# Performance work log

Hardware: AMD Instinct MI355X
Metric: run time of the kernel (lower is better)

Reference implementation:

```python
import jax, jax.numpy as jnp
import numpy as np

D_MODEL = 1024
N_HEADS = 16
D_HEAD = D_MODEL // N_HEADS
SCALE = 1.0 / (D_HEAD ** 0.5)


def _rel_shift(t):
    # Transformer-XL relative shift: pad -> view -> slice -> view. t: [b,h,q,k]
    b, h, q, k = t.shape
    padded = jnp.pad(t, ((0, 0), (0, 0), (0, 0), (1, 0)))  # [b,h,q,k+1]
    shifted = padded.reshape(b, h, k + 1, q)[:, :, 1:, :].reshape(b, h, q, k)
    return shifted


def setup_inputs() -> dict:
    key = jax.random.key(0)
    ks = jax.random.split(key, 10)
    B, T, M = 2, 1024, 1024
    J = M + T
    inp = {
        "x": jax.random.normal(ks[0], (B, T, D_MODEL), dtype=jnp.float32),
        "memory": jax.random.normal(ks[1], (B, M, D_MODEL), dtype=jnp.float32),
        "pos_emb": jax.random.normal(ks[2], (J, D_MODEL), dtype=jnp.float32),
        # nn.Linear(d, d, bias=False) weights: y = x @ W.T, W: [out, in]
        "q_w": jax.random.normal(ks[3], (D_MODEL, D_MODEL), dtype=jnp.float32) * 0.02,
        "k_w": jax.random.normal(ks[4], (D_MODEL, D_MODEL), dtype=jnp.float32) * 0.02,
        "v_w": jax.random.normal(ks[5], (D_MODEL, D_MODEL), dtype=jnp.float32) * 0.02,
        "r_w": jax.random.normal(ks[6], (D_MODEL, D_MODEL), dtype=jnp.float32) * 0.02,
        "out_w": jax.random.normal(ks[7], (D_MODEL, D_MODEL), dtype=jnp.float32) * 0.02,
        "pos_bias_u": jax.random.normal(ks[8], (N_HEADS, D_HEAD), dtype=jnp.float32) * 0.02,
        "pos_bias_v": jax.random.normal(ks[9], (N_HEADS, D_HEAD), dtype=jnp.float32) * 0.02,
    }
    return inp


def reference(x, memory, pos_emb, q_w, k_w, v_w, r_w, out_w, pos_bias_u, pos_bias_v):
    B, T, _ = x.shape
    cat = jnp.concatenate([memory, x], axis=1)  # [B, M+T, d]
    L = cat.shape[1]

    def heads(t):  # [B, time, d] -> [B, h, time, dh]
        return t.reshape(t.shape[0], t.shape[1], N_HEADS, D_HEAD).transpose(0, 2, 1, 3)

    q = heads(x @ q_w.T)      # [B,h,T,dh]
    k = heads(cat @ k_w.T)    # [B,h,L,dh]
    v = heads(cat @ v_w.T)    # [B,h,L,dh]
    r = (pos_emb @ r_w.T).reshape(-1, N_HEADS, D_HEAD).transpose(1, 0, 2)  # [h,J,dh]

    q_u = q + pos_bias_u[None, :, None, :]
    q_v = q + pos_bias_v[None, :, None, :]

    content_score = jnp.einsum('bhqd,bhkd->bhqk', q_u, k)  # [B,h,T,L]
    rel_score = jnp.einsum('bhqd,hjd->bhqj', q_v, r)        # [B,h,T,J]
    rel_score = _rel_shift(rel_score)

    scores = (content_score + rel_score) * SCALE
    attn = jax.nn.softmax(scores, axis=-1)
    out = jnp.einsum('bhqk,bhkd->bhqd', attn, v)            # [B,h,T,dh]
    out = out.transpose(0, 2, 1, 3).reshape(B, T, N_HEADS * D_HEAD)
    return out @ out_w.T
```

## Files before the change

### kernel.cpp

```cpp
#include <hip/hip_runtime.h>


typedef unsigned short u16;
typedef unsigned int u32;
typedef short bf16x8 __attribute__((ext_vector_type(8)));
typedef float f32x4 __attribute__((ext_vector_type(4)));

#define MFMA16(a, b, c) __builtin_amdgcn_mfma_f32_16x16x32_bf16(a, b, c, 0, 0, 0)

__device__ __forceinline__ u16 f2bf(float f) {
  u32 u = __float_as_uint(f);
  u32 r = (u + 0x7fffu + ((u >> 16) & 1u)) >> 16;
  return (u16)r;
}

__device__ __forceinline__ bf16x8 cvt8(float4 a, float4 b) {
  bf16x8 r;
  r[0] = (short)f2bf(a.x); r[1] = (short)f2bf(a.y);
  r[2] = (short)f2bf(a.z); r[3] = (short)f2bf(a.w);
  r[4] = (short)f2bf(b.x); r[5] = (short)f2bf(b.y);
  r[6] = (short)f2bf(b.z); r[7] = (short)f2bf(b.w);
  return r;
}

__global__ __launch_bounds__(256, 2) void gemm_qkvr(
    const float* __restrict__ x, const float* __restrict__ mem,
    const float* __restrict__ pos,
    const float* __restrict__ qw, const float* __restrict__ kw,
    const float* __restrict__ vw, const float* __restrict__ rw,
    const float* __restrict__ bu, const float* __restrict__ bv,
    u16* __restrict__ qub, u16* __restrict__ qvb, u16* __restrict__ rbuf,
    u16* __restrict__ kbuf, u16* __restrict__ vtbuf) {
  __shared__ u16 As[128 * 32], Bs[128 * 32];
  __shared__ u16 Ep[4][16 * 72];
  const int xb = blockIdx.x;
  const int bid = (xb & 7) * 96 + (xb >> 3);
  int mode, r2;
  const float* Wsrc;
  if (bid < 128)      { mode = 0; Wsrc = qw; r2 = bid; }
  else if (bid < 256) { mode = 1; Wsrc = rw; r2 = bid - 128; }
  else if (bid < 512) { mode = 2; Wsrc = kw; r2 = bid - 256; }
  else                { mode = 3; Wsrc = vw; r2 = bid - 512; }
  const int m0 = (r2 >> 3) * 128, n0 = (r2 & 7) * 128;
  const int t = threadIdx.x, lane = t & 63, wid = t >> 6;
  const int colL = lane & 15, rg = lane >> 4;
  const int wm = (wid >> 1) * 64, wn = (wid & 1) * 64;

  const float* arow[2];
  const float* wrow[2];
  int schs[2];
#pragma unroll
  for (int pass = 0; pass < 2; ++pass) {
    int slot = t + pass * 256;
    int row = slot >> 2, ch = slot & 3;
    schs[pass] = ch ^ ((row >> 1) & 3);
    int ar = m0 + row;
    if (mode == 0) {
      int b = ar >> 10;
      arow[pass] = x + ((size_t)(b * 1024 + (ar & 1023))) * 1024;
    } else if (mode == 1) {
      arow[pass] = pos + (size_t)ar * 1024;
    } else {
      int b = ar >> 11, j = ar & 2047;
      arow[pass] = (j < 1024) ? mem + ((size_t)(b * 1024 + j)) * 1024
                              : x + ((size_t)(b * 1024 + j - 1024)) * 1024;
    }
    wrow[pass] = Wsrc + (size_t)(n0 + row) * 1024;
  }

  f32x4 acc[4][4];
  f32x4 zz = {0.f, 0.f, 0.f, 0.f};
#pragma unroll
  for (int a1 = 0; a1 < 4; ++a1)
#pragma unroll
    for (int a2 = 0; a2 < 4; ++a2) acc[a1][a2] = zz;

  float4 ra[2][2], rb[2][2];
#pragma unroll
  for (int pass = 0; pass < 2; ++pass) {
    int col = schs[pass] * 8;
    ra[pass][0] = *(const float4*)(arow[pass] + col);
    ra[pass][1] = *(const float4*)(arow[pass] + col + 4);
    rb[pass][0] = *(const float4*)(wrow[pass] + col);
    rb[pass][1] = *(const float4*)(wrow[pass] + col + 4);
  }
#pragma unroll 1
  for (int kt = 0; kt < 32; ++kt) {
    __syncthreads();
#pragma unroll
    for (int pass = 0; pass < 2; ++pass) {
      int slot = t + pass * 256;
      *(bf16x8*)(As + slot * 8) = cvt8(ra[pass][0], ra[pass][1]);
      *(bf16x8*)(Bs + slot * 8) = cvt8(rb[pass][0], rb[pass][1]);
    }
    __syncthreads();
    if (kt < 31) {
#pragma unroll
      for (int pass = 0; pass < 2; ++pass) {
        int col = (kt + 1) * 32 + schs[pass] * 8;
        ra[pass][0] = *(const float4*)(arow[pass] + col);
        ra[pass][1] = *(const float4*)(arow[pass] + col + 4);
        rb[pass][0] = *(const float4*)(wrow[pass] + col);
        rb[pass][1] = *(const float4*)(wrow[pass] + col + 4);
      }
    }
    bf16x8 af[4], bfr[4];
#pragma unroll
    for (int mi = 0; mi < 4; ++mi) {
      int r = wm + mi * 16 + colL;
      af[mi] = *(const bf16x8*)(As + r * 32 + (rg ^ ((r >> 1) & 3)) * 8);
    }
#pragma unroll
    for (int ni = 0; ni < 4; ++ni) {
      int r = wn + ni * 16 + colL;
      bfr[ni] = *(const bf16x8*)(Bs + r * 32 + (rg ^ ((r >> 1) & 3)) * 8);
    }
#pragma unroll
    for (int mi = 0; mi < 4; ++mi)
#pragma unroll
      for (int ni = 0; ni < 4; ++ni)
        acc[mi][ni] = MFMA16(af[mi], bfr[ni], acc[mi][ni]);
  }

  const float sc = 0.18033688f;
  if (mode == 3) {
    u16* Ew = &Ep[wid][0];
    const int bb = m0 >> 11;
    const int j0w = (m0 + wm) & 2047;
    const int hh = (n0 + wn) >> 6;
    const size_t vb0 = (((size_t)(bb * 16 + hh) * 32 + (j0w >> 6)) * 4) * 1024;
#pragma unroll
    for (int ni = 0; ni < 4; ++ni) {
#pragma unroll
      for (int mi = 0; mi < 4; ++mi) {
        u32 lo = (u32)f2bf(acc[mi][ni][0]) | ((u32)f2bf(acc[mi][ni][1]) << 16);
        u32 hi = (u32)f2bf(acc[mi][ni][2]) | ((u32)f2bf(acc[mi][ni][3]) << 16);
        uint2 pk; pk.x = lo; pk.y = hi;
        *(uint2*)(Ew + colL * 72 + mi * 16 + rg * 4) = pk;
      }
      asm volatile("s_waitcnt lgkmcnt(0)" ::: "memory");
      const size_t vb = vb0 + (size_t)ni * 1024;
#pragma unroll
      for (int rr = 0; rr < 2; ++rr) {
        int ch = rr * 4 + rg;
        bf16x8 vv = *(const bf16x8*)(Ew + colL * 72 + ch * 8);
        *(bf16x8*)(vtbuf + vb + ch * 128 + colL * 8) = vv;
      }
      asm volatile("s_waitcnt lgkmcnt(0)" ::: "memory");
    }
    return;
  }
#pragma unroll
  for (int mi = 0; mi < 4; ++mi)
#pragma unroll
    for (int ni = 0; ni < 4; ++ni)
#pragma unroll
      for (int e = 0; e < 4; ++e) {
        int m = m0 + wm + mi * 16 + rg * 4 + e;
        int n = n0 + wn + ni * 16 + colL;
        float val = acc[mi][ni][e];
        int hh = n >> 6, dd = n & 63;
        if (mode == 0) {
          int bb = m >> 10, tq = m & 1023;
          size_t ad = (((size_t)(bb * 16 + hh)) * 1024 + tq) * 64 + dd;
          qub[ad] = f2bf((val + bu[n]) * sc);
          qvb[ad] = f2bf((val + bv[n]) * sc);
        } else if (mode == 1) {
          rbuf[((((size_t)hh * 128 + (m >> 4)) * 8 + (dd >> 3)) * 16 + (m & 15)) * 8 +
               (dd & 7)] = f2bf(val);
        } else {
          int bb = m >> 11, j = m & 2047;
          size_t bh2 = (size_t)(bb * 16 + hh);
          kbuf[(((bh2 * 128 + (j >> 4)) * 8 + (dd >> 3)) * 16 + (j & 15)) * 8 + (dd & 7)] =
              f2bf(val);
        }
      }
}

__global__ __launch_bounds__(256, 2) void attn_kernel(
    const u16* __restrict__ qu, const u16* __restrict__ qv, const u16* __restrict__ ktile,
    const u16* __restrict__ vtile, const u16* __restrict__ rtile,
    float* __restrict__ opart, float* __restrict__ lpart) {
  __shared__ float Ulds[4][3200];
  const int t = threadIdx.x;
  const int wid = t >> 6, lane = t & 63;
  const int colL = lane & 15, rg = lane >> 4;
  const int bid = ((blockIdx.x & 7) << 6) | (blockIdx.x >> 3);
  const int bh = bid >> 4;
  const int rem = bid & 15;
  const int qc = rem >> 1, ks = rem & 1;
  const int h = bh & 15;
  const int i0 = qc * 128 + wid * 32;

  const u16* qub = qu + (size_t)bh * (1024 * 64);
  const u16* qvb = qv + (size_t)bh * (1024 * 64);
  const u16* kb = ktile + (size_t)bh * (128 * 1024);
  const u16* vb = vtile + (size_t)bh * (32 * 4096);
  const u16* rb = rtile + (size_t)h * (128 * 1024);
  const int lane8 = (rg * 16 + colL) * 8;

  bf16x8 aqu0[2], aqv0[2], aqu1[2], aqv1[2];
  {
    int r0 = i0 + colL;
    int r1 = i0 + 16 + colL;
#pragma unroll
    for (int kx = 0; kx < 2; ++kx) {
      aqu0[kx] = *(const bf16x8*)(qub + (size_t)r0 * 64 + kx * 32 + rg * 8);
      aqv0[kx] = *(const bf16x8*)(qvb + (size_t)r0 * 64 + kx * 32 + rg * 8);
      aqu1[kx] = *(const bf16x8*)(qub + (size_t)r1 * 64 + kx * 32 + rg * 8);
      aqv1[kx] = *(const bf16x8*)(qvb + (size_t)r1 * 64 + kx * 32 + rg * 8);
    }
  }
  bf16x8 ones;
#pragma unroll
  for (int i = 0; i < 8; ++i) ones[i] = (short)0x3F80;

  const f32x4 zz = {0.f, 0.f, 0.f, 0.f};
  f32x4 o0[4], o1[4];
  f32x4 lacc0 = zz, lacc1 = zz;
#pragma unroll
  for (int e = 0; e < 4; ++e) { o0[e] = zz; o1[e] = zz; }
  int lb0[4], lb1[4];
#pragma unroll
  for (int e = 0; e < 4; ++e) {
    lb0[e] = (rg * 4 + e) * 99 + colL + 31;
    lb1[e] = (rg * 4 + e) * 99 + colL + 1615;
  }

  float* Uw = &Ulds[wid][0];
  u16* Pw = (u16*)Uw;

#pragma unroll 1
  for (int jt = ks * 16; jt < ks * 16 + 16; ++jt) {
    const int j0 = jt * 64;
    f32x4 s0[4], s1[4];
#pragma unroll
    for (int ni = 0; ni < 4; ++ni) {
      const u16* kp = kb + (size_t)((j0 >> 4) + ni) * 1024 + lane8;
      bf16x8 b0 = *(const bf16x8*)kp;
      bf16x8 b1 = *(const bf16x8*)(kp + 512);
      s0[ni] = zz;
      s0[ni] = MFMA16(aqu0[0], b0, s0[ni]);
      s0[ni] = MFMA16(aqu0[1], b1, s0[ni]);
      s1[ni] = zz;
      s1[ni] = MFMA16(aqu1[0], b0, s1[ni]);
      s1[ni] = MFMA16(aqu1[1], b1, s1[ni]);
    }
    const int pbase2 = j0 + 992 - i0;
    const bool mainv = (pbase2 <= 2047);
    const bool leak = (pbase2 + 94 >= 2049);
    if (mainv) {
      const int tb = pbase2 >> 4;
      bf16x8 rc[12];
#pragma unroll
      for (int uc = 0; uc < 6; ++uc) {
        int tt = tb + uc;
        tt = tt < 127 ? tt : 127;
        const u16* rp = rb + (size_t)tt * 1024 + lane8;
        rc[2 * uc] = *(const bf16x8*)rp;
        rc[2 * uc + 1] = *(const bf16x8*)(rp + 512);
      }
#pragma unroll
      for (int uc = 1; uc < 6; ++uc) {
        f32x4 ua = zz;
        ua = MFMA16(aqv0[0], rc[2 * uc], ua);
        ua = MFMA16(aqv0[1], rc[2 * uc + 1], ua);
#pragma unroll
        for (int e = 0; e < 4; ++e) Uw[(rg * 4 + e) * 100 + uc * 16 + colL] = ua[e];
      }
#pragma unroll
      for (int uc = 0; uc < 5; ++uc) {
        f32x4 ub = zz;
        ub = MFMA16(aqv1[0], rc[2 * uc], ub);
        ub = MFMA16(aqv1[1], rc[2 * uc + 1], ub);
#pragma unroll
        for (int e = 0; e < 4; ++e) Uw[(16 + rg * 4 + e) * 100 + uc * 16 + colL] = ub[e];
      }
      asm volatile("s_waitcnt lgkmcnt(0)" ::: "memory");
      const int pl0 = pbase2 + colL + 31;
      const int pl1 = pbase2 + colL + 15;
#pragma unroll
      for (int c = 0; c < 4; ++c)
#pragma unroll
        for (int e = 0; e < 4; ++e) {
          int w0e = rg * 4 + e;
          float u0 = Uw[lb0[e] + c * 16];
          float u1 = Uw[lb1[e] + c * 16];
          int p0 = pl0 + c * 16 - w0e;
          int p1 = pl1 + c * 16 - w0e;
          s0[c][e] += (p0 <= 2047) ? u0 : 0.f;
          s1[c][e] += (p1 <= 2047) ? u1 : 0.f;
        }
    }
    if (leak) {
      asm volatile("s_waitcnt lgkmcnt(0)" ::: "memory");
      bf16x8 aqs0[2], aqs1[2];
      {
        int rs0 = i0 + colL + 1;
        int rs1 = i0 + 16 + colL + 1;
        rs1 = rs1 < 1024 ? rs1 : 1023;
#pragma unroll
        for (int kx = 0; kx < 2; ++kx) {
          aqs0[kx] = *(const bf16x8*)(qvb + (size_t)rs0 * 64 + kx * 32 + rg * 8);
          aqs1[kx] = *(const bf16x8*)(qvb + (size_t)rs1 * 64 + kx * 32 + rg * 8);
        }
      }
      const int mB1 = (pbase2 - 2048) >> 4;
      const int rowL = (colL + 15) & 15;
      const int tadj = (colL > 0) ? 0 : -1;
      bf16x8 r2[12];
#pragma unroll
      for (int uc = 0; uc < 6; ++uc) {
        int tL = mB1 + uc + tadj;
        tL = tL < 0 ? 0 : (tL > 127 ? 127 : tL);
        const u16* rp = rb + (size_t)tL * 1024 + rg * 128 + rowL * 8;
        r2[2 * uc] = *(const bf16x8*)rp;
        r2[2 * uc + 1] = *(const bf16x8*)(rp + 512);
      }
#pragma unroll
      for (int uc = 1; uc < 6; ++uc) {
        f32x4 ua = zz;
        ua = MFMA16(aqs0[0], r2[2 * uc], ua);
        ua = MFMA16(aqs0[1], r2[2 * uc + 1], ua);
#pragma unroll
        for (int e = 0; e < 4; ++e) Uw[(rg * 4 + e) * 100 + uc * 16 + colL] = ua[e];
      }
#pragma unroll
      for (int uc = 0; uc < 5; ++uc) {
        f32x4 ub = zz;
        ub = MFMA16(aqs1[0], r2[2 * uc], ub);
        ub = MFMA16(aqs1[1], r2[2 * uc + 1], ub);
#pragma unroll
        for (int e = 0; e < 4; ++e) Uw[(16 + rg * 4 + e) * 100 + uc * 16 + colL] = ub[e];
      }
      asm volatile("s_waitcnt lgkmcnt(0)" ::: "memory");
      const int pl0 = pbase2 + colL + 31;
      const int pl1 = pbase2 + colL + 15;
#pragma unroll
      for (int c = 0; c < 4; ++c)
#pragma unroll
        for (int e = 0; e < 4; ++e) {
          int w0e = rg * 4 + e;
          int p0 = pl0 + c * 16 - w0e;
          int p1 = pl1 + c * 16 - w0e;
          if (p0 >= 2049) s0[c][e] += Uw[lb0[e] + c * 16];
          if (p1 >= 2049) s1[c][e] += Uw[lb1[e] + c * 16];
        }
    }
    bf16x8 vf[8];
    {
      const u16* vp0 = vb + (size_t)jt * 4096 + lane8;
#pragma unroll
      for (int ni = 0; ni < 4; ++ni) {
        vf[2 * ni] = *(const bf16x8*)(vp0 + ni * 1024);
        vf[2 * ni + 1] = *(const bf16x8*)(vp0 + ni * 1024 + 512);
      }
    }
#pragma unroll
    for (int c = 0; c < 4; ++c)
#pragma unroll
      for (int e = 0; e < 4; ++e) {
        int row = rg * 4 + e;
        int col = c * 16 + colL;
        int sw = (col >> 3) ^ (row & 7);
        float p0 = __builtin_amdgcn_exp2f(s0[c][e] - 16.0f);
        float p1 = __builtin_amdgcn_exp2f(s1[c][e] - 16.0f);
        Pw[row * 64 + sw * 8 + (colL & 7)] = f2bf(p0);
        Pw[(16 + row) * 64 + sw * 8 + (colL & 7)] = f2bf(p1);
      }
    asm volatile("s_waitcnt lgkmcnt(0)" ::: "memory");
    bf16x8 pa0[2], pa1[2];
#pragma unroll
    for (int kx = 0; kx < 2; ++kx) {
      int chunk = kx * 4 + rg;
      int sw = chunk ^ (colL & 7);
      pa0[kx] = *(const bf16x8*)(Pw + colL * 64 + sw * 8);
      pa1[kx] = *(const bf16x8*)(Pw + (16 + colL) * 64 + sw * 8);
    }
    lacc0 = MFMA16(pa0[0], ones, lacc0);
    lacc0 = MFMA16(pa0[1], ones, lacc0);
    lacc1 = MFMA16(pa1[0], ones, lacc1);
    lacc1 = MFMA16(pa1[1], ones, lacc1);
#pragma unroll
    for (int ni = 0; ni < 4; ++ni) {
      o0[ni] = MFMA16(pa0[0], vf[2 * ni], o0[ni]);
      o0[ni] = MFMA16(pa0[1], vf[2 * ni + 1], o0[ni]);
      o1[ni] = MFMA16(pa1[0], vf[2 * ni], o1[ni]);
      o1[ni] = MFMA16(pa1[1], vf[2 * ni + 1], o1[ni]);
    }
    asm volatile("" ::: "memory");
  }
  const size_t rowbase = (size_t)ks * 32768 + (size_t)bh * 1024 + i0;
#pragma unroll
  for (int c = 0; c < 4; ++c)
#pragma unroll
    for (int e = 0; e < 4; ++e) {
      int row = rg * 4 + e;
      opart[(rowbase + row) * 64 + c * 16 + colL] = o0[c][e];
      opart[(rowbase + 16 + row) * 64 + c * 16 + colL] = o1[c][e];
    }
  if (colL == 0) {
#pragma unroll
    for (int e = 0; e < 4; ++e) {
      size_t r = rowbase + rg * 4 + e;
      lpart[r] = lacc0[e];
      lpart[r + 16] = lacc1[e];
    }
  }
}

__global__ __launch_bounds__(256, 2) void gemm_out(
    const float* __restrict__ opart, const float* __restrict__ lpart,
    const float* __restrict__ ow, float* __restrict__ out) {
  __shared__ u16 As[128 * 32], Bs[128 * 32];
  const int bid = ((blockIdx.x & 7) << 4) | (blockIdx.x >> 3);
  const int mt = bid >> 3, nt = bid & 7;
  const int m0 = mt * 128, n0 = nt * 128;
  const int t = threadIdx.x, lane = t & 63, wid = t >> 6;
  const int colL = lane & 15, rg = lane >> 4;
  const int wm = (wid >> 1) * 64, wn = (wid & 1) * 64;

  int rowm[2], schs[2];
  const float* wrow[2];
#pragma unroll
  for (int pass = 0; pass < 2; ++pass) {
    int slot = t + pass * 256;
    int row = slot >> 2, ch = slot & 3;
    schs[pass] = ch ^ ((row >> 1) & 3);
    rowm[pass] = m0 + row;
    wrow[pass] = ow + (size_t)(n0 + row) * 1024;
  }

  f32x4 acc[4][4];
  f32x4 zz = {0.f, 0.f, 0.f, 0.f};
#pragma unroll
  for (int a1 = 0; a1 < 4; ++a1)
#pragma unroll
    for (int a2 = 0; a2 < 4; ++a2) acc[a1][a2] = zz;

  float4 ra[2][2], rb[2][2];
  float rl[2];
#pragma unroll
  for (int pass = 0; pass < 2; ++pass) {
    int c = schs[pass] * 8;
    int m = rowm[pass];
    int b = m >> 10, i = m & 1023;
    size_t r = ((size_t)(b * 16 + (c >> 6))) * 1024 + i;
    int dd = c & 63;
    ra[pass][0] = *(const float4*)(opart + r * 64 + dd);
    ra[pass][1] = *(const float4*)(opart + (32768 + r) * 64 + dd);
    rl[pass] = lpart[r] + lpart[32768 + r];
    rb[pass][0] = *(const float4*)(wrow[pass] + c);
    rb[pass][1] = *(const float4*)(wrow[pass] + c + 4);
  }
  float4 ra2[2][2];
#pragma unroll
  for (int pass = 0; pass < 2; ++pass) {
    int c = schs[pass] * 8;
    int m = rowm[pass];
    int b = m >> 10, i = m & 1023;
    size_t r = ((size_t)(b * 16 + (c >> 6))) * 1024 + i;
    int dd = c & 63;
    ra2[pass][0] = *(const float4*)(opart + r * 64 + dd + 4);
    ra2[pass][1] = *(const float4*)(opart + (32768 + r) * 64 + dd + 4);
  }
#pragma unroll 1
  for (int kt = 0; kt < 32; ++kt) {
    __syncthreads();
#pragma unroll
    for (int pass = 0; pass < 2; ++pass) {
      int slot = t + pass * 256;
      float inv = 1.0f / rl[pass];
      float4 lo, hi;
      lo.x = (ra[pass][0].x + ra[pass][1].x) * inv;
      lo.y = (ra[pass][0].y + ra[pass][1].y) * inv;
      lo.z = (ra[pass][0].z + ra[pass][1].z) * inv;
      lo.w = (ra[pass][0].w + ra[pass][1].w) * inv;
      hi.x = (ra2[pass][0].x + ra2[pass][1].x) * inv;
      hi.y = (ra2[pass][0].y + ra2[pass][1].y) * inv;
      hi.z = (ra2[pass][0].z + ra2[pass][1].z) * inv;
      hi.w = (ra2[pass][0].w + ra2[pass][1].w) * inv;
      *(bf16x8*)(As + slot * 8) = cvt8(lo, hi);
      *(bf16x8*)(Bs + slot * 8) = cvt8(rb[pass][0], rb[pass][1]);
    }
    __syncthreads();
    if (kt < 31) {
#pragma unroll
      for (int pass = 0; pass < 2; ++pass) {
        int c = (kt + 1) * 32 + schs[pass] * 8;
        int m = rowm[pass];
        int b = m >> 10, i = m & 1023;
        size_t r = ((size_t)(b * 16 + (c >> 6))) * 1024 + i;
        int dd = c & 63;
        ra[pass][0] = *(const float4*)(opart + r * 64 + dd);
        ra[pass][1] = *(const float4*)(opart + (32768 + r) * 64 + dd);
        ra2[pass][0] = *(const float4*)(opart + r * 64 + dd + 4);
        ra2[pass][1] = *(const float4*)(opart + (32768 + r) * 64 + dd + 4);
        rl[pass] = lpart[r] + lpart[32768 + r];
        rb[pass][0] = *(const float4*)(wrow[pass] + c);
        rb[pass][1] = *(const float4*)(wrow[pass] + c + 4);
      }
    }
    bf16x8 af[4], bfr[4];
#pragma unroll
    for (int mi = 0; mi < 4; ++mi) {
      int r = wm + mi * 16 + colL;
      af[mi] = *(const bf16x8*)(As + r * 32 + (rg ^ ((r >> 1) & 3)) * 8);
    }
#pragma unroll
    for (int ni = 0; ni < 4; ++ni) {
      int r = wn + ni * 16 + colL;
      bfr[ni] = *(const bf16x8*)(Bs + r * 32 + (rg ^ ((r >> 1) & 3)) * 8);
    }
#pragma unroll
    for (int mi = 0; mi < 4; ++mi)
#pragma unroll
      for (int ni = 0; ni < 4; ++ni)
        acc[mi][ni] = MFMA16(af[mi], bfr[ni], acc[mi][ni]);
  }
#pragma unroll
  for (int mi = 0; mi < 4; ++mi)
#pragma unroll
    for (int ni = 0; ni < 4; ++ni)
#pragma unroll
      for (int e = 0; e < 4; ++e) {
        int m = m0 + wm + mi * 16 + rg * 4 + e;
        int n = n0 + wn + ni * 16 + colL;
        out[(size_t)m * 1024 + n] = acc[mi][ni][e];
      }
}

extern "C" void kernel_launch(void* const* d_in, const int* in_sizes, int n_in,
                              void* d_out, int out_size, void* d_ws, size_t ws_size,
                              hipStream_t stream) {
  (void)in_sizes; (void)n_in; (void)out_size; (void)ws_size;
  const float* x = (const float*)d_in[0];
  const float* mem = (const float*)d_in[1];
  const float* pos = (const float*)d_in[2];
  const float* qw = (const float*)d_in[3];
  const float* kw = (const float*)d_in[4];
  const float* vw = (const float*)d_in[5];
  const float* rw = (const float*)d_in[6];
  const float* ow = (const float*)d_in[7];
  const float* bu = (const float*)d_in[8];
  const float* bv = (const float*)d_in[9];
  float* out = (float*)d_out;

  char* w = (char*)d_ws;
  float* opart = (float*)(w + 0);
  float* lpart = (float*)(w + 16777216);
  u16* qub  = (u16*)(w + 23068672);
  u16* qvb  = (u16*)(w + 27262976);
  u16* kbuf = (u16*)(w + 31457280);
  u16* vtb  = (u16*)(w + 39845888);
  u16* rbuf = (u16*)(w + 48234496);

  gemm_qkvr<<<768, 256, 0, stream>>>(x, mem, pos, qw, kw, vw, rw, bu, bv,
                                     qub, qvb, rbuf, kbuf, vtb);
  attn_kernel<<<512, 256, 0, stream>>>(qub, qvb, kbuf, vtb, rbuf, opart, lpart);
  gemm_out<<<128, 256, 0, stream>>>(opart, lpart, ow, out);
}
```

Before: 251.3 us.

## Pre-convert inputs and weights to bf16 and stage GEMM tiles via async LDS loads

Adds a prep kernel that converts the concatenated memory/x rows, the positional embeddings and all five weight matrices to bf16 in workspace. The projection GEMM and the output GEMM weight path then copy bf16 tiles straight from global memory into LDS with global_load_lds, instead of loading fp32 into registers and converting every tile. This halves the bytes each GEMM tile reads and removes conversion work from the GEMM inner loops. The cost is an extra full pass over inputs and weights, workspace regions that alias the later attention buffers, and the loss of the register-prefetch double buffering in the projection GEMM.

```diff
diff --git a/kernel.cpp b/kernel.cpp
--- a/kernel.cpp
+++ b/kernel.cpp
@@ -23,105 +23,123 @@
   return r;
 }
 
+__device__ __forceinline__ void async16(void* lds, const void* g) {
+  __builtin_amdgcn_global_load_lds(
+      (const __attribute__((address_space(1))) u32*)g,
+      (__attribute__((address_space(3))) u32*)lds, 16, 0, 0);
+}
+
+__global__ void prep_kernel(const float* __restrict__ x, const float* __restrict__ mem,
+                            const float* __restrict__ pos,
+                            const float* __restrict__ qw, const float* __restrict__ kw,
+                            const float* __restrict__ vw, const float* __restrict__ rw,
+                            const float* __restrict__ ow,
+                            u16* __restrict__ catb, u16* __restrict__ posb,
+                            u16* __restrict__ wqb, u16* __restrict__ wkb,
+                            u16* __restrict__ wvb, u16* __restrict__ wrb,
+                            u16* __restrict__ wob) {
+  const int v = blockIdx.x * 256 + threadIdx.x;
+  float4 f;
+  u16* dst;
+  if (v < 1048576) {
+    int e = v * 4;
+    int col = e & 1023;
+    int row = (e >> 10) & 2047;
+    int b = e >> 21;
+    const float* s2 = (row < 1024)
+                          ? (mem + ((size_t)(b * 1024 + row) * 1024 + col))
+                          : (x + ((size_t)(b * 1024 + (row - 1024)) * 1024 + col));
+    f = *(const float4*)s2;
+    dst = catb + (size_t)v * 4;
+  } else if (v < 1572864) {
+    int e = v - 1048576;
+    f = *(const float4*)(pos + (size_t)e * 4);
+    dst = posb + (size_t)e * 4;
+  } else {
+    int wv = v - 1572864;
+    int seg = wv >> 18;
+    int e = wv & 262143;
+    const float* src = (seg == 0) ? qw : (seg == 1) ? kw : (seg == 2) ? vw
+                                                      : (seg == 3) ? rw : ow;
+    u16* d = (seg == 0) ? wqb : (seg == 1) ? wkb : (seg == 2) ? wvb
+                                            : (seg == 3) ? wrb : wob;
+    f = *(const float4*)(src + (size_t)e * 4);
+    dst = d + (size_t)e * 4;
+  }
+  ushort4 o4;
+  o4.x = f2bf(f.x); o4.y = f2bf(f.y); o4.z = f2bf(f.z); o4.w = f2bf(f.w);
+  *(ushort4*)dst = o4;
+}
+
+__device__ __forceinline__ void gemm_core(const u16* __restrict__ A, const u16* __restrict__ W,
+                                          u16* As, u16* Bs, int m0, int n0, bool qmap,
+                                          f32x4 acc[4][4]) {
+  const int t = threadIdx.x;
+  const int lane = t & 63, wid = t >> 6;
+  const int colL = lane & 15, rg = lane >> 4;
+  const int wm = (wid >> 1) * 64, wn = (wid & 1) * 64;
+  for (int kt = 0; kt < 32; ++kt) {
+    __syncthreads();
+#pragma unroll
+    for (int pass = 0; pass < 2; ++pass) {
+      int slot = t + pass * 256;
+      int row = slot >> 2, ch = slot & 3;
+      int sch = ch ^ ((row >> 1) & 3);
+      int ar = m0 + row;
+      if (qmap) ar = ((ar >> 10) << 11) + 1024 + (ar & 1023);
+      async16(As + slot * 8, A + (size_t)ar * 1024 + kt * 32 + sch * 8);
+      async16(Bs + slot * 8, W + (size_t)(n0 + row) * 1024 + kt * 32 + sch * 8);
+    }
+    __syncthreads();
+    bf16x8 af[4], bfr[4];
+#pragma unroll
+    for (int mi = 0; mi < 4; ++mi) {
+      int r = wm + mi * 16 + colL;
+      af[mi] = *(const bf16x8*)(As + r * 32 + (rg ^ ((r >> 1) & 3)) * 8);
+    }
+#pragma unroll
+    for (int ni = 0; ni < 4; ++ni) {
+      int r = wn + ni * 16 + colL;
+      bfr[ni] = *(const bf16x8*)(Bs + r * 32 + (rg ^ ((r >> 1) & 3)) * 8);
+    }
+#pragma unroll
+    for (int mi = 0; mi < 4; ++mi)
+#pragma unroll
+      for (int ni = 0; ni < 4; ++ni)
+        acc[mi][ni] = MFMA16(af[mi], bfr[ni], acc[mi][ni]);
+  }
+}
+
 __global__ __launch_bounds__(256, 2) void gemm_qkvr(
-    const float* __restrict__ x, const float* __restrict__ mem,
-    const float* __restrict__ pos,
-    const float* __restrict__ qw, const float* __restrict__ kw,
-    const float* __restrict__ vw, const float* __restrict__ rw,
+    const u16* __restrict__ catb, const u16* __restrict__ posb,
+    const u16* __restrict__ wqb, const u16* __restrict__ wrb,
+    const u16* __restrict__ wkb, const u16* __restrict__ wvb,
     const float* __restrict__ bu, const float* __restrict__ bv,
     u16* __restrict__ qub, u16* __restrict__ qvb, u16* __restrict__ rbuf,
     u16* __restrict__ kbuf, u16* __restrict__ vtbuf) {
   __shared__ u16 As[128 * 32], Bs[128 * 32];
   __shared__ u16 Ep[4][16 * 72];
-  const int xb = blockIdx.x;
-  const int bid = (xb & 7) * 96 + (xb >> 3);
+  const int x = blockIdx.x;
+  const int bid = (x & 7) * 96 + (x >> 3);
+  const u16* A;
+  const u16* W;
   int mode, r2;
-  const float* Wsrc;
-  if (bid < 128)      { mode = 0; Wsrc = qw; r2 = bid; }
-  else if (bid < 256) { mode = 1; Wsrc = rw; r2 = bid - 128; }
-  else if (bid < 512) { mode = 2; Wsrc = kw; r2 = bid - 256; }
-  else                { mode = 3; Wsrc = vw; r2 = bid - 512; }
+  bool qmap = false;
+  if (bid < 128)      { mode = 0; A = catb; W = wqb; qmap = true; r2 = bid; }
+  else if (bid < 256) { mode = 1; A = posb; W = wrb; r2 = bid - 128; }
+  else if (bid < 512) { mode = 2; A = catb; W = wkb; r2 = bid - 256; }
+  else                { mode = 3; A = catb; W = wvb; r2 = bid - 512; }
   const int m0 = (r2 >> 3) * 128, n0 = (r2 & 7) * 128;
+  f32x4 acc[4][4];
+  f32x4 zz = {0.f, 0.f, 0.f, 0.f};
+#pragma unroll
+  for (int a1 = 0; a1 < 4; ++a1)
+#pragma unroll
+    for (int a2 = 0; a2 < 4; ++a2) acc[a1][a2] = zz;
+  gemm_core(A, W, As, Bs, m0, n0, qmap, acc);
   const int t = threadIdx.x, lane = t & 63, wid = t >> 6;
   const int colL = lane & 15, rg = lane >> 4;
   const int wm = (wid >> 1) * 64, wn = (wid & 1) * 64;
-
-  const float* arow[2];
-  const float* wrow[2];
-  int schs[2];
-#pragma unroll
-  for (int pass = 0; pass < 2; ++pass) {
-    int slot = t + pass * 256;
-    int row = slot >> 2, ch = slot & 3;
-    schs[pass] = ch ^ ((row >> 1) & 3);
-    int ar = m0 + row;
-    if (mode == 0) {
-      int b = ar >> 10;
-      arow[pass] = x + ((size_t)(b * 1024 + (ar & 1023))) * 1024;
-    } else if (mode == 1) {
-      arow[pass] = pos + (size_t)ar * 1024;
-    } else {
-      int b = ar >> 11, j = ar & 2047;
-      arow[pass] = (j < 1024) ? mem + ((size_t)(b * 1024 + j)) * 1024
-                              : x + ((size_t)(b * 1024 + j - 1024)) * 1024;
-    }
-    wrow[pass] = Wsrc + (size_t)(n0 + row) * 1024;
-  }
-
-  f32x4 acc[4][4];
-  f32x4 zz = {0.f, 0.f, 0.f, 0.f};
-#pragma unroll
-  for (int a1 = 0; a1 < 4; ++a1)
-#pragma unroll
-    for (int a2 = 0; a2 < 4; ++a2) acc[a1][a2] = zz;
-
-  float4 ra[2][2], rb[2][2];
-#pragma unroll
-  for (int pass = 0; pass < 2; ++pass) {
-    int col = schs[pass] * 8;
-    ra[pass][0] = *(const float4*)(arow[pass] + col);
-    ra[pass][1] = *(const float4*)(arow[pass] + col + 4);
-    rb[pass][0] = *(const float4*)(wrow[pass] + col);
-    rb[pass][1] = *(const float4*)(wrow[pass] + col + 4);
-  }
-#pragma unroll 1
-  for (int kt = 0; kt < 32; ++kt) {
-    __syncthreads();
-#pragma unroll
-    for (int pass = 0; pass < 2; ++pass) {
-      int slot = t + pass * 256;
-      *(bf16x8*)(As + slot * 8) = cvt8(ra[pass][0], ra[pass][1]);
-      *(bf16x8*)(Bs + slot * 8) = cvt8(rb[pass][0], rb[pass][1]);
-    }
-    __syncthreads();
-    if (kt < 31) {
-#pragma unroll
-      for (int pass = 0; pass < 2; ++pass) {
-        int col = (kt + 1) * 32 + schs[pass] * 8;
-        ra[pass][0] = *(const float4*)(arow[pass] + col);
-        ra[pass][1] = *(const float4*)(arow[pass] + col + 4);
-        rb[pass][0] = *(const float4*)(wrow[pass] + col);
-        rb[pass][1] = *(const float4*)(wrow[pass] + col + 4);
-      }
-    }
-    bf16x8 af[4], bfr[4];
-#pragma unroll
-    for (int mi = 0; mi < 4; ++mi) {
-      int r = wm + mi * 16 + colL;
-      af[mi] = *(const bf16x8*)(As + r * 32 + (rg ^ ((r >> 1) & 3)) * 8);
-    }
-#pragma unroll
-    for (int ni = 0; ni < 4; ++ni) {
-      int r = wn + ni * 16 + colL;
-      bfr[ni] = *(const bf16x8*)(Bs + r * 32 + (rg ^ ((r >> 1) & 3)) * 8);
-    }
-#pragma unroll
-    for (int mi = 0; mi < 4; ++mi)
-#pragma unroll
-      for (int ni = 0; ni < 4; ++ni)
-        acc[mi][ni] = MFMA16(af[mi], bfr[ni], acc[mi][ni]);
-  }
-
   const float sc = 0.18033688f;
   if (mode == 3) {
     u16* Ew = &Ep[wid][0];
@@ -411,7 +429,7 @@
 
 __global__ __launch_bounds__(256, 2) void gemm_out(
     const float* __restrict__ opart, const float* __restrict__ lpart,
-    const float* __restrict__ ow, float* __restrict__ out) {
+    const u16* __restrict__ wob, float* __restrict__ out) {
   __shared__ u16 As[128 * 32], Bs[128 * 32];
   const int bid = ((blockIdx.x & 7) << 4) | (blockIdx.x >> 3);
   const int mt = bid >> 3, nt = bid & 7;
@@ -420,15 +438,14 @@
   const int colL = lane & 15, rg = lane >> 4;
   const int wm = (wid >> 1) * 64, wn = (wid & 1) * 64;
 
-  int rowm[2], schs[2];
-  const float* wrow[2];
+  int rowm[2], schs[2], nrow[2];
 #pragma unroll
   for (int pass = 0; pass < 2; ++pass) {
     int slot = t + pass * 256;
     int row = slot >> 2, ch = slot & 3;
     schs[pass] = ch ^ ((row >> 1) & 3);
     rowm[pass] = m0 + row;
-    wrow[pass] = ow + (size_t)(n0 + row) * 1024;
+    nrow[pass] = n0 + row;
   }
 
   f32x4 acc[4][4];
@@ -438,7 +455,7 @@
 #pragma unroll
     for (int a2 = 0; a2 < 4; ++a2) acc[a1][a2] = zz;
 
-  float4 ra[2][2], rb[2][2];
+  float4 ra[2][2], ra2[2][2];
   float rl[2];
 #pragma unroll
   for (int pass = 0; pass < 2; ++pass) {
@@ -449,20 +466,9 @@
     int dd = c & 63;
     ra[pass][0] = *(const float4*)(opart + r * 64 + dd);
     ra[pass][1] = *(const float4*)(opart + (32768 + r) * 64 + dd);
-    rl[pass] = lpart[r] + lpart[32768 + r];
-    rb[pass][0] = *(const float4*)(wrow[pass] + c);
-    rb[pass][1] = *(const float4*)(wrow[pass] + c + 4);
-  }
-  float4 ra2[2][2];
-#pragma unroll
-  for (int pass = 0; pass < 2; ++pass) {
-    int c = schs[pass] * 8;
-    int m = rowm[pass];
-    int b = m >> 10, i = m & 1023;
-    size_t r = ((size_t)(b * 16 + (c >> 6))) * 1024 + i;
-    int dd = c & 63;
     ra2[pass][0] = *(const float4*)(opart + r * 64 + dd + 4);
     ra2[pass][1] = *(const float4*)(opart + (32768 + r) * 64 + dd + 4);
+    rl[pass] = lpart[r] + lpart[32768 + r];
   }
 #pragma unroll 1
   for (int kt = 0; kt < 32; ++kt) {
@@ -470,6 +476,7 @@
 #pragma unroll
     for (int pass = 0; pass < 2; ++pass) {
       int slot = t + pass * 256;
+      async16(Bs + slot * 8, wob + (size_t)nrow[pass] * 1024 + kt * 32 + schs[pass] * 8);
       float inv = 1.0f / rl[pass];
       float4 lo, hi;
       lo.x = (ra[pass][0].x + ra[pass][1].x) * inv;
@@ -481,7 +488,6 @@
       hi.z = (ra2[pass][0].z + ra2[pass][1].z) * inv;
       hi.w = (ra2[pass][0].w + ra2[pass][1].w) * inv;
       *(bf16x8*)(As + slot * 8) = cvt8(lo, hi);
-      *(bf16x8*)(Bs + slot * 8) = cvt8(rb[pass][0], rb[pass][1]);
     }
     __syncthreads();
     if (kt < 31) {
@@ -497,8 +503,6 @@
         ra2[pass][0] = *(const float4*)(opart + r * 64 + dd + 4);
         ra2[pass][1] = *(const float4*)(opart + (32768 + r) * 64 + dd + 4);
         rl[pass] = lpart[r] + lpart[32768 + r];
-        rb[pass][0] = *(const float4*)(wrow[pass] + c);
-        rb[pass][1] = *(const float4*)(wrow[pass] + c + 4);
       }
     }
     bf16x8 af[4], bfr[4];
@@ -547,16 +551,25 @@
   float* out = (float*)d_out;
 
   char* w = (char*)d_ws;
-  float* opart = (float*)(w + 0);
-  float* lpart = (float*)(w + 16777216);
+  u16* catb = (u16*)(w + 0);
+  u16* posb = (u16*)(w + 8388608);
+  u16* wqb  = (u16*)(w + 12582912);
+  u16* wkb  = (u16*)(w + 14680064);
+  u16* wvb  = (u16*)(w + 16777216);
+  u16* wrb  = (u16*)(w + 18874368);
+  u16* wob  = (u16*)(w + 20971520);
   u16* qub  = (u16*)(w + 23068672);
   u16* qvb  = (u16*)(w + 27262976);
   u16* kbuf = (u16*)(w + 31457280);
   u16* vtb  = (u16*)(w + 39845888);
   u16* rbuf = (u16*)(w + 48234496);
-
-  gemm_qkvr<<<768, 256, 0, stream>>>(x, mem, pos, qw, kw, vw, rw, bu, bv,
+  float* opart = (float*)(w + 0);
+  float* lpart = (float*)(w + 16777216);
+
+  prep_kernel<<<11264, 256, 0, stream>>>(x, mem, pos, qw, kw, vw, rw, ow,
+                                         catb, posb, wqb, wkb, wvb, wrb, wob);
+  gemm_qkvr<<<768, 256, 0, stream>>>(catb, posb, wqb, wrb, wkb, wvb, bu, bv,
                                      qub, qvb, rbuf, kbuf, vtb);
   attn_kernel<<<512, 256, 0, stream>>>(qub, qvb, kbuf, vtb, rbuf, opart, lpart);
-  gemm_out<<<128, 256, 0, stream>>>(opart, lpart, ow, out);
-}
+  gemm_out<<<128, 256, 0, stream>>>(opart, lpart, wob, out);
+}
```

Measured after the change: 248.2 us. Within noise of the previous version (-1.2%).
